# Performance work log

Measured on AMD Instinct MI355X. Metric: run time of the kernel, lower is better.

Reference implementation:

```python
import jax, jax.numpy as jnp
import numpy as np

N, D, C = 1024, 512, 85742
S, M, EPS = 64.0, 0.5, 1e-07  # arcface defaults


def setup_inputs() -> dict:
    key = jax.random.key(0)
    k1, k2, k3 = jax.random.split(key, 3)
    x = jax.random.normal(k1, (N, D), dtype=jnp.float32)
    W = jax.random.normal(k2, (C, D), dtype=jnp.float32) * 0.05
    labels = jax.random.randint(k3, (N,), 0, C, dtype=jnp.int64)
    return {"x": x, "W": W, "labels": labels, "positive": 1}


def reference(x, W, labels, positive):
    # L2-normalize x rows (torch F.normalize semantics, eps=1e-12).
    # NOTE: the original torch code's weight-normalization loop is a no-op,
    # so W is used unnormalized, faithfully reproduced here.
    xn = x / jnp.maximum(jnp.linalg.norm(x, axis=1, keepdims=True), 1e-12)
    wf = xn @ W.T  # [N, C] cosine-like logits (W unnormalized)
    if not positive:
        return wf
    rows = jnp.arange(wf.shape[0])
    target = wf[rows, labels]  # diagonal gather
    # arcface margin: s * cos(acos(clamped) + m)
    numerator = S * jnp.cos(jnp.arccos(jnp.clip(target, -1.0 + EPS, 1.0 - EPS)) + M)
    # masked exp-sum over non-target classes (replaces Python-loop excl)
    exp_all = jnp.exp(S * wf)
    excl_sum = jnp.sum(exp_all, axis=1) - exp_all[rows, labels]
    denominator = jnp.exp(numerator) + excl_sum
    L = numerator - jnp.log(denominator)
    return (wf, -jnp.mean(L))
```

## Files before the change

kernel.cpp:

```cpp
#include <hip/hip_runtime.h>
#include <hip/hip_bf16.h>

#define NROW 1024
#define DDIM 512
#define CDIM 85742
#define SSC 64.0f
#define MARG 0.5f
#define AEPS 1e-7f

typedef __attribute__((ext_vector_type(8))) short bf16x8;
typedef __attribute__((ext_vector_type(4))) float f32x4;

__device__ __forceinline__ void async_ld16(const void* g, void* l) {
  __builtin_amdgcn_global_load_lds((const __attribute__((address_space(1))) void*)g,
                                   (__attribute__((address_space(3))) void*)l, 16, 0, 0);
}

__global__ void row_normalize(const float* __restrict__ x, __hip_bfloat16* __restrict__ xn,
                              float* __restrict__ rowsum) {
  const int row = blockIdx.x;
  const int lane = threadIdx.x;
  if (lane == 0) rowsum[row] = 0.0f;
  const float4* xr = (const float4*)(x + (size_t)row * DDIM);
  float4 a = xr[lane * 2 + 0];
  float4 b = xr[lane * 2 + 1];
  float ss = a.x * a.x + a.y * a.y + a.z * a.z + a.w * a.w +
             b.x * b.x + b.y * b.y + b.z * b.z + b.w * b.w;
#pragma unroll
  for (int o = 32; o >= 1; o >>= 1) ss += __shfl_xor(ss, o);
  const float inv = 1.0f / fmaxf(sqrtf(ss), 1e-12f);
  __hip_bfloat16 t[8];
  t[0] = __float2bfloat16(a.x * inv); t[1] = __float2bfloat16(a.y * inv);
  t[2] = __float2bfloat16(a.z * inv); t[3] = __float2bfloat16(a.w * inv);
  t[4] = __float2bfloat16(b.x * inv); t[5] = __float2bfloat16(b.y * inv);
  t[6] = __float2bfloat16(b.z * inv); t[7] = __float2bfloat16(b.w * inv);
  *(bf16x8*)(xn + (size_t)row * DDIM + lane * 8) = *(bf16x8*)t;
}

__device__ __forceinline__ bf16x8 cvt8(f32x4 lo, f32x4 hi) {
  __hip_bfloat16 t[8];
  t[0] = __float2bfloat16(lo.x); t[1] = __float2bfloat16(lo.y);
  t[2] = __float2bfloat16(lo.z); t[3] = __float2bfloat16(lo.w);
  t[4] = __float2bfloat16(hi.x); t[5] = __float2bfloat16(hi.y);
  t[6] = __float2bfloat16(hi.z); t[7] = __float2bfloat16(hi.w);
  return *(bf16x8*)t;
}

__global__ __launch_bounds__(256) void gemm_loss(const __hip_bfloat16* __restrict__ A,
                                                 const float* __restrict__ W,
                                                 float* __restrict__ wf,
                                                 float* __restrict__ rowsum) {
  const int id = blockIdx.x;
  const int xcd = id & 7;
  const int s = id >> 3;
  const int ctile = xcd * 84 + (s >> 3);
  if (ctile >= 670) return;
  const int mtile = s & 7;

  __shared__ __hip_bfloat16 As[128 * 32];
  __shared__ float Bs[128 * 32];
  const int tid = threadIdx.x;
  const int lane = tid & 63;
  const int wav = tid >> 6;
  const int wm = wav >> 1, wn = wav & 1;
  const int row0 = mtile * 128;
  const int col0 = ctile * 128;
  const int lr = lane & 15, lq = lane >> 4;
  const int waveBase = tid & ~63;

  f32x4 acc[4][4] = {};

  for (int k0 = 0; k0 < DDIM; k0 += 32) {
#pragma unroll
    for (int q = 0; q < 2; ++q) {
      const int chunk = q * 256 + tid;
      const int r = chunk >> 2, kc = chunk & 3;
      async_ld16(A + ((size_t)(row0 + r) * DDIM + k0 + kc * 8),
                 As + (q * 256 + waveBase) * 8);
    }
#pragma unroll
    for (int q = 0; q < 4; ++q) {
      const int chunk = q * 256 + tid;
      const int r = chunk >> 3, kc = chunk & 7;
      const int kcs = kc ^ (r & 7);
      int gr = col0 + r;
      gr = gr < CDIM ? gr : CDIM - 1;
      async_ld16(W + ((size_t)gr * DDIM + k0 + kcs * 4),
                 Bs + (q * 256 + waveBase) * 4);
    }
    __syncthreads();

    bf16x8 af[4], bfr[4];
#pragma unroll
    for (int i = 0; i < 4; ++i)
      af[i] = *(const bf16x8*)(As + (wm * 64 + i * 16 + lr) * 32 + lq * 8);
#pragma unroll
    for (int j = 0; j < 4; ++j) {
      const int br = wn * 64 + j * 16 + lr;
      const int s0 = (2 * lq) ^ (br & 7);
      const int s1 = (2 * lq + 1) ^ (br & 7);
      f32x4 lo = *(const f32x4*)(Bs + br * 32 + s0 * 4);
      f32x4 hi = *(const f32x4*)(Bs + br * 32 + s1 * 4);
      bfr[j] = cvt8(lo, hi);
    }
#pragma unroll
    for (int i = 0; i < 4; ++i)
#pragma unroll
      for (int j = 0; j < 4; ++j)
        acc[i][j] = __builtin_amdgcn_mfma_f32_16x16x32_bf16(af[i], bfr[j], acc[i][j], 0, 0, 0);
    __syncthreads();
  }

#pragma unroll
  for (int i = 0; i < 4; ++i) {
    const int rb = row0 + wm * 64 + i * 16 + lq * 4;
#pragma unroll
    for (int r = 0; r < 4; ++r) {
      const int grow = rb + r;
      float esum = 0.f;
#pragma unroll
      for (int j = 0; j < 4; ++j) {
        const int gcol = col0 + wn * 64 + j * 16 + lr;
        const float v = acc[i][j][r];
        if (gcol < CDIM) {
          wf[(size_t)grow * CDIM + gcol] = v;
          esum += __expf(SSC * v);
        }
      }
      esum += __shfl_xor(esum, 1);
      esum += __shfl_xor(esum, 2);
      esum += __shfl_xor(esum, 4);
      esum += __shfl_xor(esum, 8);
      if (lr == 0) atomicAdd(rowsum + grow, esum);
    }
  }
}

__global__ void finalize(const float* __restrict__ wf, const float* __restrict__ rowsum,
                         const int* __restrict__ labels, float* __restrict__ out_loss) {
  const int i = threadIdx.x;
  const int lab = labels[i];
  const float tgt = wf[(size_t)i * CDIM + lab];
  const float tc = fminf(fmaxf(tgt, -1.0f + AEPS), 1.0f - AEPS);
  const float num = SSC * cosf(acosf(tc) + MARG);
  const float excl = rowsum[i] - __expf(SSC * tgt);
  float L = num - logf(__expf(num) + excl);
#pragma unroll
  for (int o = 32; o >= 1; o >>= 1) L += __shfl_xor(L, o);
  __shared__ float red[16];
  if ((i & 63) == 0) red[i >> 6] = L;
  __syncthreads();
  if (i < 64) {
    float v = (i < 16) ? red[i] : 0.f;
#pragma unroll
    for (int o = 8; o >= 1; o >>= 1) v += __shfl_xor(v, o);
    if (i == 0) out_loss[0] = -v * (1.0f / NROW);
  }
}

extern "C" void kernel_launch(void* const* d_in, const int* in_sizes, int n_in,
                              void* d_out, int out_size, void* d_ws, size_t ws_size,
                              hipStream_t stream) {
  const float* x = (const float*)d_in[0];
  const float* W = (const float*)d_in[1];
  const int* labels = (const int*)d_in[2];
  float* out = (float*)d_out;

  float* rowsum = (float*)d_ws;
  __hip_bfloat16* xn = (__hip_bfloat16*)((char*)d_ws + 4096);

  row_normalize<<<NROW, 64, 0, stream>>>(x, xn, rowsum);
  gemm_loss<<<672 * 8, 256, 0, stream>>>(xn, W, out, rowsum);
  finalize<<<1, 1024, 0, stream>>>(out, rowsum, labels, out + (size_t)NROW * CDIM);
}
```

Measured before the change: 660.0 us.

## Pre-convert W to bf16 in a separate pass and swizzle LDS tiles

Adds a kernel that converts W from fp32 to bf16 into workspace once per call. The GEMM then loads bf16 B tiles without per-tile conversion, halving B traffic per reuse across the 8 M-tiles. It also adds an XOR swizzle to the A/B LDS layout and uses nontemporal stores for the large wf output. The extra pass reads W once and writes a half-size copy, and the bf16 path only runs when the workspace is large enough.

New measurement: 659.2 us. About the same (-0.1%).

```diff
diff --git a/kernel.cpp b/kernel.cpp
--- a/kernel.cpp
+++ b/kernel.cpp
@@ -14,6 +14,15 @@
 __device__ __forceinline__ void async_ld16(const void* g, void* l) {
   __builtin_amdgcn_global_load_lds((const __attribute__((address_space(1))) void*)g,
                                    (__attribute__((address_space(3))) void*)l, 16, 0, 0);
+}
+
+__device__ __forceinline__ bf16x8 cvt8(f32x4 lo, f32x4 hi) {
+  __hip_bfloat16 t[8];
+  t[0] = __float2bfloat16(lo.x); t[1] = __float2bfloat16(lo.y);
+  t[2] = __float2bfloat16(lo.z); t[3] = __float2bfloat16(lo.w);
+  t[4] = __float2bfloat16(hi.x); t[5] = __float2bfloat16(hi.y);
+  t[6] = __float2bfloat16(hi.z); t[7] = __float2bfloat16(hi.w);
+  return *(bf16x8*)t;
 }
 
 __global__ void row_normalize(const float* __restrict__ x, __hip_bfloat16* __restrict__ xn,
@@ -37,16 +46,20 @@
   *(bf16x8*)(xn + (size_t)row * DDIM + lane * 8) = *(bf16x8*)t;
 }
 
-__device__ __forceinline__ bf16x8 cvt8(f32x4 lo, f32x4 hi) {
-  __hip_bfloat16 t[8];
-  t[0] = __float2bfloat16(lo.x); t[1] = __float2bfloat16(lo.y);
-  t[2] = __float2bfloat16(lo.z); t[3] = __float2bfloat16(lo.w);
-  t[4] = __float2bfloat16(hi.x); t[5] = __float2bfloat16(hi.y);
-  t[6] = __float2bfloat16(hi.z); t[7] = __float2bfloat16(hi.w);
-  return *(bf16x8*)t;
-}
-
+__global__ void w_to_bf16(const float* __restrict__ W, __hip_bfloat16* __restrict__ Wb) {
+  const size_t total = (size_t)CDIM * DDIM / 8;
+  const size_t stride = (size_t)gridDim.x * blockDim.x;
+  for (size_t i = (size_t)blockIdx.x * blockDim.x + threadIdx.x; i < total; i += stride) {
+    const f32x4* p = (const f32x4*)(W + i * 8);
+    f32x4 a = __builtin_nontemporal_load(p);
+    f32x4 b = __builtin_nontemporal_load(p + 1);
+    *(bf16x8*)(Wb + i * 8) = cvt8(a, b);
+  }
+}
+
+template <int WB16>
 __global__ __launch_bounds__(256) void gemm_loss(const __hip_bfloat16* __restrict__ A,
+                                                 const __hip_bfloat16* __restrict__ Wb,
                                                  const float* __restrict__ W,
                                                  float* __restrict__ wf,
                                                  float* __restrict__ rowsum) {
@@ -57,8 +70,11 @@
   if (ctile >= 670) return;
   const int mtile = s & 7;
 
-  __shared__ __hip_bfloat16 As[128 * 32];
-  __shared__ float Bs[128 * 32];
+  __shared__ __align__(16) char smem[WB16 ? (8192 + 8192) : (8192 + 16384)];
+  __hip_bfloat16* As = (__hip_bfloat16*)smem;
+  __hip_bfloat16* Bs16 = (__hip_bfloat16*)(smem + 8192);
+  float* Bs32 = (float*)(smem + 8192);
+
   const int tid = threadIdx.x;
   const int lane = tid & 63;
   const int wav = tid >> 6;
@@ -75,33 +91,57 @@
     for (int q = 0; q < 2; ++q) {
       const int chunk = q * 256 + tid;
       const int r = chunk >> 2, kc = chunk & 3;
-      async_ld16(A + ((size_t)(row0 + r) * DDIM + k0 + kc * 8),
+      const int kcs = kc ^ (r & 3);
+      async_ld16(A + ((size_t)(row0 + r) * DDIM + k0 + kcs * 8),
                  As + (q * 256 + waveBase) * 8);
     }
-#pragma unroll
-    for (int q = 0; q < 4; ++q) {
-      const int chunk = q * 256 + tid;
-      const int r = chunk >> 3, kc = chunk & 7;
-      const int kcs = kc ^ (r & 7);
-      int gr = col0 + r;
-      gr = gr < CDIM ? gr : CDIM - 1;
-      async_ld16(W + ((size_t)gr * DDIM + k0 + kcs * 4),
-                 Bs + (q * 256 + waveBase) * 4);
+    if constexpr (WB16) {
+#pragma unroll
+      for (int q = 0; q < 2; ++q) {
+        const int chunk = q * 256 + tid;
+        const int r = chunk >> 2, kc = chunk & 3;
+        const int kcs = kc ^ (r & 3);
+        int gr = col0 + r;
+        gr = gr < CDIM ? gr : CDIM - 1;
+        async_ld16(Wb + ((size_t)gr * DDIM + k0 + kcs * 8),
+                   Bs16 + (q * 256 + waveBase) * 8);
+      }
+    } else {
+#pragma unroll
+      for (int q = 0; q < 4; ++q) {
+        const int chunk = q * 256 + tid;
+        const int r = chunk >> 3, kc = chunk & 7;
+        const int kcs = kc ^ (r & 7);
+        int gr = col0 + r;
+        gr = gr < CDIM ? gr : CDIM - 1;
+        async_ld16(W + ((size_t)gr * DDIM + k0 + kcs * 4),
+                   Bs32 + (q * 256 + waveBase) * 4);
+      }
     }
     __syncthreads();
 
     bf16x8 af[4], bfr[4];
 #pragma unroll
-    for (int i = 0; i < 4; ++i)
-      af[i] = *(const bf16x8*)(As + (wm * 64 + i * 16 + lr) * 32 + lq * 8);
-#pragma unroll
-    for (int j = 0; j < 4; ++j) {
-      const int br = wn * 64 + j * 16 + lr;
-      const int s0 = (2 * lq) ^ (br & 7);
-      const int s1 = (2 * lq + 1) ^ (br & 7);
-      f32x4 lo = *(const f32x4*)(Bs + br * 32 + s0 * 4);
-      f32x4 hi = *(const f32x4*)(Bs + br * 32 + s1 * 4);
-      bfr[j] = cvt8(lo, hi);
+    for (int i = 0; i < 4; ++i) {
+      const int ar = wm * 64 + i * 16 + lr;
+      af[i] = *(const bf16x8*)(As + ar * 32 + (lq ^ (ar & 3)) * 8);
+    }
+    if constexpr (WB16) {
+#pragma unroll
+      for (int j = 0; j < 4; ++j) {
+        const int br = wn * 64 + j * 16 + lr;
+        bfr[j] = *(const bf16x8*)(Bs16 + br * 32 + (lq ^ (br & 3)) * 8);
+      }
+    } else {
+#pragma unroll
+      for (int j = 0; j < 4; ++j) {
+        const int br = wn * 64 + j * 16 + lr;
+        const int s0 = (2 * lq) ^ (br & 7);
+        const int s1 = (2 * lq + 1) ^ (br & 7);
+        f32x4 lo = *(const f32x4*)(Bs32 + br * 32 + s0 * 4);
+        f32x4 hi = *(const f32x4*)(Bs32 + br * 32 + s1 * 4);
+        bfr[j] = cvt8(lo, hi);
+      }
     }
 #pragma unroll
     for (int i = 0; i < 4; ++i)
@@ -123,7 +163,7 @@
         const int gcol = col0 + wn * 64 + j * 16 + lr;
         const float v = acc[i][j][r];
         if (gcol < CDIM) {
-          wf[(size_t)grow * CDIM + gcol] = v;
+          __builtin_nontemporal_store(v, wf + (size_t)grow * CDIM + gcol);
           esum += __expf(SSC * v);
         }
       }
@@ -168,8 +208,16 @@
 
   float* rowsum = (float*)d_ws;
   __hip_bfloat16* xn = (__hip_bfloat16*)((char*)d_ws + 4096);
+  const size_t wb_off = 4096 + (size_t)NROW * DDIM * 2;
+  const size_t need = wb_off + (size_t)CDIM * DDIM * 2;
+  __hip_bfloat16* Wb = (__hip_bfloat16*)((char*)d_ws + wb_off);
 
   row_normalize<<<NROW, 64, 0, stream>>>(x, xn, rowsum);
-  gemm_loss<<<672 * 8, 256, 0, stream>>>(xn, W, out, rowsum);
+  if (ws_size >= need) {
+    w_to_bf16<<<2048, 256, 0, stream>>>(W, Wb);
+    gemm_loss<1><<<672 * 8, 256, 0, stream>>>(xn, Wb, nullptr, out, rowsum);
+  } else {
+    gemm_loss<0><<<672 * 8, 256, 0, stream>>>(xn, nullptr, W, out, rowsum);
+  }
   finalize<<<1, 1024, 0, stream>>>(out, rowsum, labels, out + (size_t)NROW * CDIM);
 }
```

## Pre-convert W to bf16, double-buffer LDS, and enlarge M tile to 256

Applied to the files above, without the earlier changes.

A prep kernel now converts W from fp32 to bf16 in workspace, fused with the x row normalization. The GEMM then loads bf16 B tiles instead of fp32 ones and no longer converts inside the loop. The GEMM also uses 512-thread blocks covering 256 rows, so each W tile is reused across twice as many rows, and it double-buffers the LDS stages to overlap loads with MFMA. This costs an extra full pass over W (read fp32, write bf16) and more workspace, in exchange for halving W traffic in the GEMM and doing fewer conversions overall.

After: 645.4 us. 2.2% less time.

```diff
diff --git a/kernel.cpp b/kernel.cpp
--- a/kernel.cpp
+++ b/kernel.cpp
@@ -14,27 +14,6 @@
 __device__ __forceinline__ void async_ld16(const void* g, void* l) {
   __builtin_amdgcn_global_load_lds((const __attribute__((address_space(1))) void*)g,
                                    (__attribute__((address_space(3))) void*)l, 16, 0, 0);
-}
-
-__global__ void row_normalize(const float* __restrict__ x, __hip_bfloat16* __restrict__ xn,
-                              float* __restrict__ rowsum) {
-  const int row = blockIdx.x;
-  const int lane = threadIdx.x;
-  if (lane == 0) rowsum[row] = 0.0f;
-  const float4* xr = (const float4*)(x + (size_t)row * DDIM);
-  float4 a = xr[lane * 2 + 0];
-  float4 b = xr[lane * 2 + 1];
-  float ss = a.x * a.x + a.y * a.y + a.z * a.z + a.w * a.w +
-             b.x * b.x + b.y * b.y + b.z * b.z + b.w * b.w;
-#pragma unroll
-  for (int o = 32; o >= 1; o >>= 1) ss += __shfl_xor(ss, o);
-  const float inv = 1.0f / fmaxf(sqrtf(ss), 1e-12f);
-  __hip_bfloat16 t[8];
-  t[0] = __float2bfloat16(a.x * inv); t[1] = __float2bfloat16(a.y * inv);
-  t[2] = __float2bfloat16(a.z * inv); t[3] = __float2bfloat16(a.w * inv);
-  t[4] = __float2bfloat16(b.x * inv); t[5] = __float2bfloat16(b.y * inv);
-  t[6] = __float2bfloat16(b.z * inv); t[7] = __float2bfloat16(b.w * inv);
-  *(bf16x8*)(xn + (size_t)row * DDIM + lane * 8) = *(bf16x8*)t;
 }
 
 __device__ __forceinline__ bf16x8 cvt8(f32x4 lo, f32x4 hi) {
@@ -46,68 +25,117 @@
   return *(bf16x8*)t;
 }
 
-__global__ __launch_bounds__(256) void gemm_loss(const __hip_bfloat16* __restrict__ A,
-                                                 const float* __restrict__ W,
-                                                 float* __restrict__ wf,
-                                                 float* __restrict__ rowsum) {
+__global__ __launch_bounds__(256) void prep(const float* __restrict__ x,
+                                            const float* __restrict__ W,
+                                            __hip_bfloat16* __restrict__ xn,
+                                            __hip_bfloat16* __restrict__ Wb,
+                                            float* __restrict__ rowsum) {
+  const int bid = blockIdx.x;
+  if (bid >= 2048) {
+    const int row = ((bid - 2048) << 2) + (threadIdx.x >> 6);
+    const int lane = threadIdx.x & 63;
+    if (lane == 0) rowsum[row] = 0.0f;
+    const float4* xr = (const float4*)(x + (size_t)row * DDIM);
+    float4 a = xr[lane * 2 + 0];
+    float4 b = xr[lane * 2 + 1];
+    float ss = a.x * a.x + a.y * a.y + a.z * a.z + a.w * a.w +
+               b.x * b.x + b.y * b.y + b.z * b.z + b.w * b.w;
+#pragma unroll
+    for (int o = 32; o >= 1; o >>= 1) ss += __shfl_xor(ss, o);
+    const float inv = 1.0f / fmaxf(sqrtf(ss), 1e-12f);
+    __hip_bfloat16 t[8];
+    t[0] = __float2bfloat16(a.x * inv); t[1] = __float2bfloat16(a.y * inv);
+    t[2] = __float2bfloat16(a.z * inv); t[3] = __float2bfloat16(a.w * inv);
+    t[4] = __float2bfloat16(b.x * inv); t[5] = __float2bfloat16(b.y * inv);
+    t[6] = __float2bfloat16(b.z * inv); t[7] = __float2bfloat16(b.w * inv);
+    *(bf16x8*)(xn + (size_t)row * DDIM + lane * 8) = *(bf16x8*)t;
+    return;
+  }
+  const size_t total = (size_t)CDIM * DDIM / 8;
+  const size_t stride = (size_t)2048 * 256;
+  for (size_t i = (size_t)bid * 256 + threadIdx.x; i < total; i += stride) {
+    const f32x4* p = (const f32x4*)(W + i * 8);
+    f32x4 a = __builtin_nontemporal_load(p);
+    f32x4 b = __builtin_nontemporal_load(p + 1);
+    *(bf16x8*)(Wb + i * 8) = cvt8(a, b);
+  }
+}
+
+__global__ __launch_bounds__(512, 4) void gemm_loss(const __hip_bfloat16* __restrict__ A,
+                                                    const __hip_bfloat16* __restrict__ Wb,
+                                                    float* __restrict__ wf,
+                                                    float* __restrict__ rowsum) {
   const int id = blockIdx.x;
   const int xcd = id & 7;
   const int s = id >> 3;
-  const int ctile = xcd * 84 + (s >> 3);
+  const int ctile = xcd * 84 + (s >> 2);
   if (ctile >= 670) return;
-  const int mtile = s & 7;
-
-  __shared__ __hip_bfloat16 As[128 * 32];
-  __shared__ float Bs[128 * 32];
+  const int mtile = s & 3;
+
+  __shared__ __align__(16) char smem[2 * 24576];
+
   const int tid = threadIdx.x;
   const int lane = tid & 63;
   const int wav = tid >> 6;
   const int wm = wav >> 1, wn = wav & 1;
-  const int row0 = mtile * 128;
+  const int row0 = mtile * 256;
   const int col0 = ctile * 128;
   const int lr = lane & 15, lq = lane >> 4;
   const int waveBase = tid & ~63;
 
   f32x4 acc[4][4] = {};
 
-  for (int k0 = 0; k0 < DDIM; k0 += 32) {
+  auto STAGE = [&](int b, int k0) {
+    __hip_bfloat16* As = (__hip_bfloat16*)(smem + b * 24576);
+    __hip_bfloat16* Bs = (__hip_bfloat16*)(smem + b * 24576 + 16384);
 #pragma unroll
     for (int q = 0; q < 2; ++q) {
-      const int chunk = q * 256 + tid;
+      const int chunk = q * 512 + tid;
       const int r = chunk >> 2, kc = chunk & 3;
-      async_ld16(A + ((size_t)(row0 + r) * DDIM + k0 + kc * 8),
-                 As + (q * 256 + waveBase) * 8);
-    }
-#pragma unroll
-    for (int q = 0; q < 4; ++q) {
-      const int chunk = q * 256 + tid;
-      const int r = chunk >> 3, kc = chunk & 7;
-      const int kcs = kc ^ (r & 7);
+      const int kcs = kc ^ (r & 3);
+      async_ld16(A + ((size_t)(row0 + r) * DDIM + k0 + kcs * 8),
+                 As + (q * 512 + waveBase) * 8);
+    }
+    {
+      const int r = tid >> 2, kc = tid & 3;
+      const int kcs = kc ^ (r & 3);
       int gr = col0 + r;
       gr = gr < CDIM ? gr : CDIM - 1;
-      async_ld16(W + ((size_t)gr * DDIM + k0 + kcs * 4),
-                 Bs + (q * 256 + waveBase) * 4);
-    }
-    __syncthreads();
-
+      async_ld16(Wb + ((size_t)gr * DDIM + k0 + kcs * 8),
+                 Bs + waveBase * 8);
+    }
+  };
+
+  auto COMPUTE = [&](int b) {
+    const __hip_bfloat16* As = (const __hip_bfloat16*)(smem + b * 24576);
+    const __hip_bfloat16* Bs = (const __hip_bfloat16*)(smem + b * 24576 + 16384);
     bf16x8 af[4], bfr[4];
 #pragma unroll
-    for (int i = 0; i < 4; ++i)
-      af[i] = *(const bf16x8*)(As + (wm * 64 + i * 16 + lr) * 32 + lq * 8);
+    for (int i = 0; i < 4; ++i) {
+      const int ar = wm * 64 + i * 16 + lr;
+      af[i] = *(const bf16x8*)(As + ar * 32 + (lq ^ (ar & 3)) * 8);
+    }
 #pragma unroll
     for (int j = 0; j < 4; ++j) {
       const int br = wn * 64 + j * 16 + lr;
-      const int s0 = (2 * lq) ^ (br & 7);
-      const int s1 = (2 * lq + 1) ^ (br & 7);
-      f32x4 lo = *(const f32x4*)(Bs + br * 32 + s0 * 4);
-      f32x4 hi = *(const f32x4*)(Bs + br * 32 + s1 * 4);
-      bfr[j] = cvt8(lo, hi);
+      bfr[j] = *(const bf16x8*)(Bs + br * 32 + (lq ^ (br & 3)) * 8);
     }
 #pragma unroll
     for (int i = 0; i < 4; ++i)
 #pragma unroll
       for (int j = 0; j < 4; ++j)
         acc[i][j] = __builtin_amdgcn_mfma_f32_16x16x32_bf16(af[i], bfr[j], acc[i][j], 0, 0, 0);
+  };
+
+  STAGE(0, 0);
+  __syncthreads();
+#pragma unroll 1
+  for (int k0 = 0; k0 < DDIM; k0 += 64) {
+    STAGE(1, k0 + 32);
+    COMPUTE(0);
+    __syncthreads();
+    if (k0 + 64 < DDIM) STAGE(0, k0 + 64);
+    COMPUTE(1);
     __syncthreads();
   }
 
@@ -168,8 +196,10 @@
 
   float* rowsum = (float*)d_ws;
   __hip_bfloat16* xn = (__hip_bfloat16*)((char*)d_ws + 4096);
-
-  row_normalize<<<NROW, 64, 0, stream>>>(x, xn, rowsum);
-  gemm_loss<<<672 * 8, 256, 0, stream>>>(xn, W, out, rowsum);
+  const size_t wb_off = 4096 + (size_t)NROW * DDIM * 2;
+  __hip_bfloat16* Wb = (__hip_bfloat16*)((char*)d_ws + wb_off);
+
+  prep<<<2304, 256, 0, stream>>>(x, W, xn, Wb, rowsum);
+  gemm_loss<<<2688, 512, 0, stream>>>(xn, Wb, out, rowsum);
   finalize<<<1, 1024, 0, stream>>>(out, rowsum, labels, out + (size_t)NROW * CDIM);
 }
```
